# Performance work log

Hardware: AMD Instinct MI355X
Metric: run time of the kernel (lower is better)

The kernel has to match this reference:

```python
import jax, jax.numpy as jnp
import numpy as np

K = 512
DIM = 64


def setup_inputs() -> dict:
    key = jax.random.key(0)
    kx, ke = jax.random.split(key)
    x = jax.random.normal(kx, (64, 64, 32, 32), dtype=jnp.float32)  # (b, d, h, w)
    codebook = jax.random.normal(ke, (K, DIM), dtype=jnp.float32)  # nn.Embedding weight
    return {"x": x, "codebook": codebook}


def reference(x, codebook):
    b, d, h, w = x.shape
    # (b, d, h*w) -> (b, h*w, d)
    flat = jnp.transpose(x.reshape(b, d, h * w), (0, 2, 1))  # (b, n, d)
    x2 = jnp.sum(flat * flat, axis=-1, keepdims=True)              # (b, n, 1)
    e2 = jnp.sum(codebook * codebook, axis=-1)                     # (k,)
    xe = jnp.einsum('bnd,kd->bnk', flat, codebook)                 # (b, n, k)
    dist = x2 - 2.0 * xe + e2                                      # (b, n, k)
    idx = jnp.argmin(dist, axis=-1)                                # (b, n)
    quant = codebook[idx]                                          # (b, n, d) gather
    # straight-through estimator
    quant_st = flat + jax.lax.stop_gradient(quant - flat)
    out = jnp.transpose(quant_st, (0, 2, 1)).reshape(b, d, h, w)
    return out
```

## Files before the change

kernel.cpp:

```cpp
#include <hip/hip_runtime.h>

#define KCODES 512
#define DIM    64
#define NVEC   65536
#define TAU    0.05f

typedef __attribute__((ext_vector_type(8))) short   short8;
typedef __attribute__((ext_vector_type(4))) float   f32x4;

#define GLOAD_LDS16(gp, lp) __builtin_amdgcn_global_load_lds(                  \
    (const __attribute__((address_space(1))) unsigned int*)(gp),               \
    (__attribute__((address_space(3))) unsigned int*)(lp), 16, 0, 0)

static __device__ __forceinline__ unsigned f2bfu(float f) {
    unsigned u = __builtin_bit_cast(unsigned, f);
    u += 0x7fffu + ((u >> 16) & 1u);
    return u >> 16;
}

__global__ void prep_kernel(const float* __restrict__ cb,
                            unsigned short* __restrict__ cbt,
                            float* __restrict__ e2q) {
    if (blockIdx.x < 128) {
        const int g   = blockIdx.x * 64 + threadIdx.x;
        const int s   = g >> 10;
        const int rem = g & 1023;
        const int h   = rem >> 9;
        const int qd  = (rem >> 6) & 7;
        const int cl  = rem & 63;
        const float* src = cb + (size_t)(s * 64 + cl) * DIM + qd * 8;
        short8 v;
#pragma unroll
        for (int j = 0; j < 8; ++j) {
            float f = src[j];
            unsigned u = __builtin_bit_cast(unsigned, f);
            if (h == 0) {
                v[j] = (short)(u >> 16);
            } else {
                float hi = __builtin_bit_cast(float, u & 0xFFFF0000u);
                v[j] = (short)f2bfu(f - hi);
            }
        }
        *(short8*)(cbt + (size_t)g * 8) = v;
    } else {
        const int k = blockIdx.x - 128;
        float v = cb[k * DIM + threadIdx.x];
        double p = (double)v * (double)v;
#pragma unroll
        for (int off = 32; off > 0; off >>= 1) p += __shfl_down(p, off, 64);
        if (threadIdx.x == 0) e2q[k] = (float)(0.5 * p + 256.0);
    }
}

__launch_bounds__(256, 4)
__global__ void vq_main(const float* __restrict__ x,
                        const float* __restrict__ cb,
                        const unsigned short* __restrict__ cbt,
                        const float* __restrict__ e2q,
                        float* __restrict__ out) {
    __shared__ __align__(16) unsigned short sA[2][8192];
    __shared__ float sE2[KCODES];
    __shared__ int   s_i1[64], s_i2[64], s_flag[64], s_win[64];

    const int tid  = threadIdx.x;
    const int wave = tid >> 6;
    const int lane = tid & 63;
    const int quad = lane >> 4;
    const int l16  = lane & 15;

    const int v0    = blockIdx.x * 64;
    const int b     = v0 >> 10;
    const int nbase = v0 & 1023;
    const float* xb = x + (size_t)b * 65536;

#pragma unroll
    for (int r = 0; r < 4; ++r) {
        const int g = tid + r * 256;
        GLOAD_LDS16(cbt + (size_t)g * 8, sA[0] + (size_t)g * 8);
    }

    short8 Bh[2], Bl[2];
    {
        const int n_g = nbase + wave * 16 + l16;
#pragma unroll
        for (int ko = 0; ko < 2; ++ko) {
#pragma unroll
            for (int j = 0; j < 8; ++j) {
                const int d = quad * 8 + j + ko * 32;
                float f = -xb[(size_t)d * 1024 + n_g];
                unsigned u = __builtin_bit_cast(unsigned, f);
                float hi = __builtin_bit_cast(float, u & 0xFFFF0000u);
                Bh[ko][j] = (short)(u >> 16);
                Bl[ko][j] = (short)f2bfu(f - hi);
            }
        }
    }

    if (tid < 128) *(f32x4*)(sE2 + tid * 4) = *(const f32x4*)(e2q + tid * 4);
    __syncthreads();

    float f1 = 1e30f, f2_ = 1e30f;
    int   i1 = 0,     i2_ = 0;

#pragma unroll 1
    for (int s = 0; s < 8; ++s) {
        if (s < 7) {
#pragma unroll
            for (int r = 0; r < 4; ++r) {
                const int g = tid + r * 256;
                GLOAD_LDS16(cbt + (size_t)((s + 1) * 1024 + g) * 8,
                            sA[(s + 1) & 1] + (size_t)g * 8);
            }
        }

        const unsigned short* buf = sA[s & 1];
#pragma unroll
        for (int st = 0; st < 4; ++st) {
            const int cbase = s * 64 + st * 16;
            const int roff  = quad * 64 + st * 16 + l16;
            short8 A00 = *(const short8*)(buf + (size_t)(      roff) * 8);
            short8 A01 = *(const short8*)(buf + (size_t)(256 + roff) * 8);
            short8 A10 = *(const short8*)(buf + (size_t)(512 + roff) * 8);
            short8 A11 = *(const short8*)(buf + (size_t)(768 + roff) * 8);
            f32x4  e2v = *(const f32x4*)(sE2 + cbase + quad * 4);

            f32x4 acc = e2v;
            acc = __builtin_amdgcn_mfma_f32_16x16x32_bf16(A00, Bh[0], acc, 0, 0, 0);
            acc = __builtin_amdgcn_mfma_f32_16x16x32_bf16(A01, Bh[1], acc, 0, 0, 0);
            acc = __builtin_amdgcn_mfma_f32_16x16x32_bf16(A00, Bl[0], acc, 0, 0, 0);
            acc = __builtin_amdgcn_mfma_f32_16x16x32_bf16(A01, Bl[1], acc, 0, 0, 0);
            acc = __builtin_amdgcn_mfma_f32_16x16x32_bf16(A10, Bh[0], acc, 0, 0, 0);
            acc = __builtin_amdgcn_mfma_f32_16x16x32_bf16(A11, Bh[1], acc, 0, 0, 0);

#pragma unroll
            for (int r = 0; r < 4; ++r) {
                float dd = acc[r];
                int   id = cbase + quad * 4 + r;
                bool  c1 = dd < f1;
                bool  c2 = dd < f2_;
                i2_ = c1 ? i1 : (c2 ? id : i2_);
                f2_ = __builtin_amdgcn_fmed3f(f1, dd, f2_);
                i1  = c1 ? id : i1;
                f1  = fminf(f1, dd);
            }
        }
        if (s < 7) __syncthreads();
    }

    {
#pragma unroll
        for (int delta = 16; delta <= 32; delta <<= 1) {
            float of1 = __shfl_xor(f1, delta, 64);
            int   oi1 = __shfl_xor(i1, delta, 64);
            float of2 = __shfl_xor(f2_, delta, 64);
            int   oi2 = __shfl_xor(i2_, delta, 64);
            bool o1_first = (of1 < f1) || (of1 == f1 && oi1 < i1);
            if (o1_first) {
                bool keep = (f1 < of2) || (f1 == of2 && i1 < oi2);
                f2_ = keep ? f1 : of2;
                i2_ = keep ? i1 : oi2;
                f1 = of1; i1 = oi1;
            } else {
                bool o1_second = (of1 < f2_) || (of1 == f2_ && oi1 < i2_);
                if (o1_second) { f2_ = of1; i2_ = oi1; }
            }
        }
        if (quad == 0) {
            const int vl = wave * 16 + l16;
            s_win[vl]  = i1;
            s_i1[vl]   = i1;
            s_i2[vl]   = i2_;
            s_flag[vl] = (f2_ - f1) < TAU;
        }
    }
    __syncthreads();

    {
        const int vec = tid >> 2, sub = tid & 3;
        if (s_flag[vec]) {
            const int i1c = s_i1[vec], i2c = s_i2[vec];
            const float* xr = xb + nbase + vec;
            const float* r1 = cb + (size_t)i1c * DIM;
            const float* r2 = cb + (size_t)i2c * DIM;
            double D1 = 0.0, D2 = 0.0;
#pragma unroll 4
            for (int i = 0; i < 16; ++i) {
                const int d = sub + 4 * i;
                double xd = (double)xr[(size_t)d * 1024];
                double t1 = xd - (double)r1[d]; D1 += t1 * t1;
                double t2 = xd - (double)r2[d]; D2 += t2 * t2;
            }
            D1 += __shfl_down(D1, 2, 64); D1 += __shfl_down(D1, 1, 64);
            D2 += __shfl_down(D2, 2, 64); D2 += __shfl_down(D2, 1, 64);
            if (sub == 0) {
                if (D2 < D1 || (D2 == D1 && i2c < i1c)) s_win[vec] = i2c;
            }
        }
    }
    __syncthreads();

    {
        const int n    = tid & 63;
        const int dgrp = tid >> 6;
        const float4* crow = (const float4*)(cb + (size_t)s_win[n] * DIM);
        float* op = out + (size_t)b * 65536 + nbase + n;
#pragma unroll
        for (int i = 0; i < 4; ++i) {
            const int d0 = dgrp * 16 + i * 4;
            float4 val = crow[d0 >> 2];
            op[(size_t)(d0 + 0) * 1024] = val.x;
            op[(size_t)(d0 + 1) * 1024] = val.y;
            op[(size_t)(d0 + 2) * 1024] = val.z;
            op[(size_t)(d0 + 3) * 1024] = val.w;
        }
    }
}

extern "C" void kernel_launch(void* const* d_in, const int* in_sizes, int n_in,
                              void* d_out, int out_size, void* d_ws, size_t ws_size,
                              hipStream_t stream) {
    const float* x  = (const float*)d_in[0];
    const float* cb = (const float*)d_in[1];
    float* out = (float*)d_out;

    unsigned short* cbt = (unsigned short*)d_ws;
    float*          e2q = (float*)(cbt + 8192 * 8);

    prep_kernel<<<640, 64, 0, stream>>>(cb, cbt, e2q);
    vq_main<<<NVEC / 64, 256, 0, stream>>>(x, cb, cbt, e2q, out);
}
```

Measured before the change: 90.42 us.

## Split codebook across wave pairs, each wave handling two vector tiles

Waves now split the code dimension in halves and each handles 32 vectors (two 16-vector tiles), so every A fragment loaded from LDS is reused by two MFMA chains. This halves LDS reads of codebook fragments per MFMA and gives two independent accumulator chains for ILP. It costs extra B registers and an extra LDS-based merge of top-2 results between wave pairs plus a barrier.

```diff
diff --git a/kernel.cpp b/kernel.cpp
--- a/kernel.cpp
+++ b/kernel.cpp
@@ -60,13 +60,17 @@
                         float* __restrict__ out) {
     __shared__ __align__(16) unsigned short sA[2][8192];
     __shared__ float sE2[KCODES];
+    __shared__ float s_mf1[2][64], s_mf2[2][64];
+    __shared__ int   s_mi1[2][64], s_mi2[2][64];
     __shared__ int   s_i1[64], s_i2[64], s_flag[64], s_win[64];
 
-    const int tid  = threadIdx.x;
-    const int wave = tid >> 6;
-    const int lane = tid & 63;
-    const int quad = lane >> 4;
-    const int l16  = lane & 15;
+    const int tid   = threadIdx.x;
+    const int wave  = tid >> 6;
+    const int lane  = tid & 63;
+    const int vhalf = wave >> 1;
+    const int chalf = wave & 1;
+    const int quad  = lane >> 4;
+    const int l16   = lane & 15;
 
     const int v0    = blockIdx.x * 64;
     const int b     = v0 >> 10;
@@ -79,9 +83,10 @@
         GLOAD_LDS16(cbt + (size_t)g * 8, sA[0] + (size_t)g * 8);
     }
 
-    short8 Bh[2], Bl[2];
-    {
-        const int n_g = nbase + wave * 16 + l16;
+    short8 Bh[2][2], Bl[2][2];
+#pragma unroll
+    for (int nt = 0; nt < 2; ++nt) {
+        const int n_g = nbase + vhalf * 32 + nt * 16 + l16;
 #pragma unroll
         for (int ko = 0; ko < 2; ++ko) {
 #pragma unroll
@@ -90,8 +95,8 @@
                 float f = -xb[(size_t)d * 1024 + n_g];
                 unsigned u = __builtin_bit_cast(unsigned, f);
                 float hi = __builtin_bit_cast(float, u & 0xFFFF0000u);
-                Bh[ko][j] = (short)(u >> 16);
-                Bl[ko][j] = (short)f2bfu(f - hi);
+                Bh[nt][ko][j] = (short)(u >> 16);
+                Bl[nt][ko][j] = (short)f2bfu(f - hi);
             }
         }
     }
@@ -99,8 +104,8 @@
     if (tid < 128) *(f32x4*)(sE2 + tid * 4) = *(const f32x4*)(e2q + tid * 4);
     __syncthreads();
 
-    float f1 = 1e30f, f2_ = 1e30f;
-    int   i1 = 0,     i2_ = 0;
+    float f1[2] = {1e30f, 1e30f}, f2_[2] = {1e30f, 1e30f};
+    int   i1[2] = {0, 0},         i2_[2] = {0, 0};
 
 #pragma unroll 1
     for (int s = 0; s < 8; ++s) {
@@ -115,7 +120,8 @@
 
         const unsigned short* buf = sA[s & 1];
 #pragma unroll
-        for (int st = 0; st < 4; ++st) {
+        for (int j = 0; j < 2; ++j) {
+            const int st    = chalf * 2 + j;
             const int cbase = s * 64 + st * 16;
             const int roff  = quad * 64 + st * 16 + l16;
             short8 A00 = *(const short8*)(buf + (size_t)(      roff) * 8);
@@ -124,54 +130,78 @@
             short8 A11 = *(const short8*)(buf + (size_t)(768 + roff) * 8);
             f32x4  e2v = *(const f32x4*)(sE2 + cbase + quad * 4);
 
-            f32x4 acc = e2v;
-            acc = __builtin_amdgcn_mfma_f32_16x16x32_bf16(A00, Bh[0], acc, 0, 0, 0);
-            acc = __builtin_amdgcn_mfma_f32_16x16x32_bf16(A01, Bh[1], acc, 0, 0, 0);
-            acc = __builtin_amdgcn_mfma_f32_16x16x32_bf16(A00, Bl[0], acc, 0, 0, 0);
-            acc = __builtin_amdgcn_mfma_f32_16x16x32_bf16(A01, Bl[1], acc, 0, 0, 0);
-            acc = __builtin_amdgcn_mfma_f32_16x16x32_bf16(A10, Bh[0], acc, 0, 0, 0);
-            acc = __builtin_amdgcn_mfma_f32_16x16x32_bf16(A11, Bh[1], acc, 0, 0, 0);
-
-#pragma unroll
-            for (int r = 0; r < 4; ++r) {
-                float dd = acc[r];
-                int   id = cbase + quad * 4 + r;
-                bool  c1 = dd < f1;
-                bool  c2 = dd < f2_;
-                i2_ = c1 ? i1 : (c2 ? id : i2_);
-                f2_ = __builtin_amdgcn_fmed3f(f1, dd, f2_);
-                i1  = c1 ? id : i1;
-                f1  = fminf(f1, dd);
+#pragma unroll
+            for (int nt = 0; nt < 2; ++nt) {
+                f32x4 acc = e2v;
+                acc = __builtin_amdgcn_mfma_f32_16x16x32_bf16(A00, Bh[nt][0], acc, 0, 0, 0);
+                acc = __builtin_amdgcn_mfma_f32_16x16x32_bf16(A01, Bh[nt][1], acc, 0, 0, 0);
+                acc = __builtin_amdgcn_mfma_f32_16x16x32_bf16(A00, Bl[nt][0], acc, 0, 0, 0);
+                acc = __builtin_amdgcn_mfma_f32_16x16x32_bf16(A01, Bl[nt][1], acc, 0, 0, 0);
+                acc = __builtin_amdgcn_mfma_f32_16x16x32_bf16(A10, Bh[nt][0], acc, 0, 0, 0);
+                acc = __builtin_amdgcn_mfma_f32_16x16x32_bf16(A11, Bh[nt][1], acc, 0, 0, 0);
+
+#pragma unroll
+                for (int r = 0; r < 4; ++r) {
+                    float dd = acc[r];
+                    int   id = cbase + quad * 4 + r;
+                    bool  c1 = dd < f1[nt];
+                    bool  c2 = dd < f2_[nt];
+                    i2_[nt] = c1 ? i1[nt] : (c2 ? id : i2_[nt]);
+                    f2_[nt] = __builtin_amdgcn_fmed3f(f1[nt], dd, f2_[nt]);
+                    i1[nt]  = c1 ? id : i1[nt];
+                    f1[nt]  = fminf(f1[nt], dd);
+                }
             }
         }
         if (s < 7) __syncthreads();
     }
 
-    {
+#pragma unroll
+    for (int nt = 0; nt < 2; ++nt) {
+        float F1 = f1[nt], F2 = f2_[nt];
+        int   I1 = i1[nt], I2 = i2_[nt];
 #pragma unroll
         for (int delta = 16; delta <= 32; delta <<= 1) {
-            float of1 = __shfl_xor(f1, delta, 64);
-            int   oi1 = __shfl_xor(i1, delta, 64);
-            float of2 = __shfl_xor(f2_, delta, 64);
-            int   oi2 = __shfl_xor(i2_, delta, 64);
-            bool o1_first = (of1 < f1) || (of1 == f1 && oi1 < i1);
+            float of1 = __shfl_xor(F1, delta, 64);
+            int   oi1 = __shfl_xor(I1, delta, 64);
+            float of2 = __shfl_xor(F2, delta, 64);
+            int   oi2 = __shfl_xor(I2, delta, 64);
+            bool o1_first = (of1 < F1) || (of1 == F1 && oi1 < I1);
             if (o1_first) {
-                bool keep = (f1 < of2) || (f1 == of2 && i1 < oi2);
-                f2_ = keep ? f1 : of2;
-                i2_ = keep ? i1 : oi2;
-                f1 = of1; i1 = oi1;
+                bool keep = (F1 < of2) || (F1 == of2 && I1 < oi2);
+                F2 = keep ? F1 : of2;
+                I2 = keep ? I1 : oi2;
+                F1 = of1; I1 = oi1;
             } else {
-                bool o1_second = (of1 < f2_) || (of1 == f2_ && oi1 < i2_);
-                if (o1_second) { f2_ = of1; i2_ = oi1; }
+                bool o1_second = (of1 < F2) || (of1 == F2 && oi1 < I2);
+                if (o1_second) { F2 = of1; I2 = oi1; }
             }
         }
         if (quad == 0) {
-            const int vl = wave * 16 + l16;
-            s_win[vl]  = i1;
-            s_i1[vl]   = i1;
-            s_i2[vl]   = i2_;
-            s_flag[vl] = (f2_ - f1) < TAU;
-        }
+            const int vl = vhalf * 32 + nt * 16 + l16;
+            s_mf1[chalf][vl] = F1; s_mi1[chalf][vl] = I1;
+            s_mf2[chalf][vl] = F2; s_mi2[chalf][vl] = I2;
+        }
+    }
+    __syncthreads();
+
+    if (tid < 64) {
+        float F1 = s_mf1[0][tid], F2 = s_mf2[0][tid];
+        int   I1 = s_mi1[0][tid], I2 = s_mi2[0][tid];
+        float of1 = s_mf1[1][tid], of2 = s_mf2[1][tid];
+        int   oi1 = s_mi1[1][tid], oi2 = s_mi2[1][tid];
+        bool o1_first = (of1 < F1) || (of1 == F1 && oi1 < I1);
+        if (o1_first) {
+            bool keep = (F1 < of2) || (F1 == of2 && I1 < oi2);
+            F2 = keep ? F1 : of2;  I2 = keep ? I1 : oi2;
+            F1 = of1; I1 = oi1;
+        } else if ((of1 < F2) || (of1 == F2 && oi1 < I2)) {
+            F2 = of1; I2 = oi1;
+        }
+        s_win[tid]  = I1;
+        s_i1[tid]   = I1;
+        s_i2[tid]   = I2;
+        s_flag[tid] = (F2 - F1) < TAU;
     }
     __syncthreads();
 
```

After: 93.60 us. 1.04x slower.
